# Kernel tuning notes

Measured on AMD Instinct MI355X. Metric: run time of the kernel, lower is better.

Reference implementation:

```python
import jax, jax.numpy as jnp
import numpy as np

SIZE = 384  # output resolution
SCALE = (0.8, 1.0)


def _bilinear_crop_resize(img, cs, top, left):
    """img: [C,H,W]; cs/top/left: int32 scalars. Crop [top:top+cs, left:left+cs],
    resize to SIZE x SIZE with bilinear, align_corners=False (PyTorch semantics)."""
    csf = cs.astype(jnp.float32)
    # source coords within the crop, clamped like PyTorch (src = max(src,0), upper bounded)
    coords = (jnp.arange(SIZE, dtype=jnp.float32) + 0.5) * (csf / SIZE) - 0.5
    coords = jnp.clip(coords, 0.0, csf - 1.0)
    i0 = jnp.floor(coords).astype(jnp.int32)
    i1 = jnp.minimum(i0 + 1, cs - 1)
    w = coords - i0.astype(jnp.float32)  # [SIZE]
    y0, y1 = i0 + top, i1 + top
    x0, x1 = i0 + left, i1 + left
    wy, wx = w[:, None], w[None, :]
    g = lambda yy, xx: img[:, yy[:, None], xx[None, :]]  # [C,SIZE,SIZE]
    return (g(y0, x0) * (1 - wy) * (1 - wx)
            + g(y0, x1) * (1 - wy) * wx
            + g(y1, x0) * wy * (1 - wx)
            + g(y1, x1) * wy * wx)


def _nearest_crop_resize(msk, cs, top, left):
    """msk: [1,H,W]. PyTorch mode='nearest': src_idx = floor(dst * in/out)."""
    idx = jnp.floor(jnp.arange(SIZE, dtype=jnp.float32) * cs.astype(jnp.float32) / SIZE).astype(jnp.int32)
    idx = jnp.minimum(idx, cs - 1)
    y, x = idx + top, idx + left
    return msk[:, y[:, None], x[None, :]]


def setup_inputs() -> dict:
    key = jax.random.key(0)
    k1, k2, k3, k4, k5 = jax.random.split(key, 5)
    B, C, H, W = 32, 3, 512, 512
    image = jax.random.normal(k1, (B, C, H, W), dtype=jnp.float32)
    mask = (jax.random.uniform(k2, (B, 1, H, W)) > 0.5).astype(jnp.float32)
    scale = jax.random.uniform(k3, (B,), minval=SCALE[0], maxval=SCALE[1])
    crop_size = (scale * min(H, W)).astype(jnp.int32)
    max_y = (H - crop_size).astype(jnp.float32)
    max_x = (W - crop_size).astype(jnp.float32)
    top = jnp.where(max_y > 0, jnp.floor(jax.random.uniform(k4, (B,)) * max_y), 0.0).astype(jnp.int32)
    left = jnp.where(max_x > 0, jnp.floor(jax.random.uniform(k5, (B,)) * max_x), 0.0).astype(jnp.int32)
    return {"image": image, "mask": mask, "crop_size": crop_size, "top": top, "left": left}


def reference(image, mask, crop_size, top, left):
    img_out = jax.vmap(_bilinear_crop_resize)(image, crop_size, top, left)
    msk_out = jax.vmap(_nearest_crop_resize)(mask, crop_size, top, left)
    return img_out, msk_out
```

## Files before the change

kernel.cpp:

```cpp
#include <hip/hip_runtime.h>


constexpr int OUT = 384;
constexpr int H = 512;
constexpr int W = 512;
constexpr int B = 32;
constexpr int C = 3;
constexpr int RPB = 4;
constexpr int GPB = OUT / RPB;
constexpr int SW  = 128;
constexpr int NSTRIPE = OUT / SW;
constexpr int NSLOT = 6;
constexpr int LROWS = C * NSLOT;
constexpr int NW  = 176;
constexpr int NCH = NW / 4;
constexpr int TOT_CHUNK = LROWS * NCH;
constexpr int NBLK = B * GPB * NSTRIPE;
constexpr int BPX  = NBLK / 8;

typedef float f32x4 __attribute__((ext_vector_type(4)));

__global__ __launch_bounds__(128, 6) void rrc_pair_kernel(
    const float* __restrict__ image,
    const float* __restrict__ mask,
    const int* __restrict__ crop_size,
    const int* __restrict__ top,
    const int* __restrict__ left,
    float* __restrict__ img_out,
    float* __restrict__ msk_out)
{
    __shared__ float lds[LROWS * NW + 8];

    const int hw = blockIdx.x;
    const int logical = (hw & 7) * BPX + (hw >> 3);
    const int b   = logical / (GPB * NSTRIPE);
    const int rem = logical % (GPB * NSTRIPE);
    const int grp = rem / NSTRIPE;
    const int st  = rem % NSTRIPE;
    const int i0  = grp * RPB;
    const int c0  = st * SW;
    const int tid = (int)threadIdx.x;
    const int j   = c0 + tid;

    const int cs = crop_size[b];
    const int t  = top[b];
    const int l  = left[b];
    const float csf = (float)cs;
    const float s   = csf / (float)OUT;

    float cy0 = ((float)i0 + 0.5f) * s - 0.5f;
    cy0 = fminf(fmaxf(cy0, 0.0f), csf - 1.0f);
    const int base_y = (int)floorf(cy0);

    float cx0 = ((float)c0 + 0.5f) * s - 0.5f;
    cx0 = fminf(fmaxf(cx0, 0.0f), csf - 1.0f);
    const int gx0 = (int)floorf(cx0);
    const int cbg = min(l + gx0, W - NW) & ~3;

    const float* imgb = image + (size_t)b * C * H * W;

    #pragma unroll
    for (int rd = 0; rd < 7; ++rd) {
        const int q = rd * 128 + tid;
        if (q < TOT_CHUNK) {
            const int r   = q / NCH;
            const int col = (q - r * NCH) * 4;
            const int c    = r / NSLOT;
            const int slot = r - c * NSLOT;
            const int y = min(t + base_y + slot, H - 1);
            const float* src = imgb + ((size_t)(c * H + y)) * W + cbg + col;
            __builtin_amdgcn_global_load_lds(
                (const __attribute__((address_space(1))) void*)src,
                (__attribute__((address_space(3))) void*)&lds[q * 4],
                16, 0, 0);
        }
    }
    if (tid < 8) lds[LROWS * NW + tid] = 0.0f;

    float cx = ((float)j + 0.5f) * s - 0.5f;
    cx = fminf(fmaxf(cx, 0.0f), csf - 1.0f);
    const int   ix0 = (int)floorf(cx);
    const float wx  = cx - (float)ix0;
    const int   xoff = l + ix0 - cbg;

    const int mx = min((j * cs) / OUT, cs - 1) + l;

    float mval[RPB];
    #pragma unroll
    for (int r4 = 0; r4 < RPB; ++r4) {
        int my = min(((i0 + r4) * cs) / OUT, cs - 1);
        mval[r4] = mask[((size_t)b * H + (size_t)(my + t)) * W + mx];
    }

    __syncthreads();

    #pragma unroll
    for (int r4 = 0; r4 < RPB; ++r4) {
        const int i = i0 + r4;
        float cy = ((float)i + 0.5f) * s - 0.5f;
        cy = fminf(fmaxf(cy, 0.0f), csf - 1.0f);
        int   iy0 = (int)floorf(cy);
        int   iy1 = min(iy0 + 1, cs - 1);
        float wy  = cy - (float)iy0;
        const int slot0 = iy0 - base_y;
        const int slot1 = min(iy1 - base_y, NSLOT - 1);

        const float w00 = (1.0f - wy) * (1.0f - wx);
        const float w01 = (1.0f - wy) * wx;
        const float w10 = wy * (1.0f - wx);
        const float w11 = wy * wx;

        const size_t o_base = (size_t)b * C * OUT * OUT + (size_t)i * OUT + (size_t)j;

        #pragma unroll
        for (int c = 0; c < C; ++c) {
            const float* rA = &lds[(c * NSLOT + slot0) * NW + xoff];
            const float* rB = &lds[(c * NSLOT + slot1) * NW + xoff];
            float v00 = rA[0], v01 = rA[1];
            float v10 = rB[0], v11 = rB[1];
            float rr = v00 * w00 + v01 * w01 + v10 * w10 + v11 * w11;
            __builtin_nontemporal_store(rr, img_out + o_base + (size_t)c * OUT * OUT);
        }
        __builtin_nontemporal_store(mval[r4],
            msk_out + (size_t)b * OUT * OUT + (size_t)i * OUT + (size_t)j);
    }
}

extern "C" void kernel_launch(void* const* d_in, const int* in_sizes, int n_in,
                              void* d_out, int out_size, void* d_ws, size_t ws_size,
                              hipStream_t stream) {
    const float* image = (const float*)d_in[0];
    const float* mask  = (const float*)d_in[1];
    const int* cs      = (const int*)d_in[2];
    const int* top     = (const int*)d_in[3];
    const int* left    = (const int*)d_in[4];

    float* img_out = (float*)d_out;
    float* msk_out = img_out + (size_t)B * C * OUT * OUT;

    dim3 block(128);
    dim3 grid(NBLK);
    hipLaunchKernelGGL(rrc_pair_kernel, grid, block, 0, stream,
                       image, mask, cs, top, left, img_out, msk_out);
}
```

Baseline: 31.79 us.

## Halve rows per block and have each thread emit two adjacent pixels

Each block now covers 2 output rows instead of 4, so it stages 4 source rows per channel instead of 6. The 128 threads are split into two 64-lane halves, one per row, and each thread computes two neighbouring columns and writes them with float2 stores. Occupancy is raised to 8 blocks per CU. This doubles the grid size and re-reads more overlapping source rows across blocks, in exchange for smaller LDS use, more blocks resident per CU and wider stores.

```diff
diff --git a/kernel.cpp b/kernel.cpp
--- a/kernel.cpp
+++ b/kernel.cpp
@@ -6,11 +6,11 @@
 constexpr int W = 512;
 constexpr int B = 32;
 constexpr int C = 3;
-constexpr int RPB = 4;
+constexpr int RPB = 2;
 constexpr int GPB = OUT / RPB;
 constexpr int SW  = 128;
 constexpr int NSTRIPE = OUT / SW;
-constexpr int NSLOT = 6;
+constexpr int NSLOT = 4;
 constexpr int LROWS = C * NSLOT;
 constexpr int NW  = 176;
 constexpr int NCH = NW / 4;
@@ -18,9 +18,9 @@
 constexpr int NBLK = B * GPB * NSTRIPE;
 constexpr int BPX  = NBLK / 8;
 
-typedef float f32x4 __attribute__((ext_vector_type(4)));
+typedef float f32x2 __attribute__((ext_vector_type(2)));
 
-__global__ __launch_bounds__(128, 6) void rrc_pair_kernel(
+__global__ __launch_bounds__(128, 8) void rrc_pair_kernel(
     const float* __restrict__ image,
     const float* __restrict__ mask,
     const int* __restrict__ crop_size,
@@ -29,7 +29,7 @@
     float* __restrict__ img_out,
     float* __restrict__ msk_out)
 {
-    __shared__ float lds[LROWS * NW + 8];
+    __shared__ float lds[LROWS * NW];
 
     const int hw = blockIdx.x;
     const int logical = (hw & 7) * BPX + (hw >> 3);
@@ -40,7 +40,6 @@
     const int i0  = grp * RPB;
     const int c0  = st * SW;
     const int tid = (int)threadIdx.x;
-    const int j   = c0 + tid;
 
     const int cs = crop_size[b];
     const int t  = top[b];
@@ -60,7 +59,7 @@
     const float* imgb = image + (size_t)b * C * H * W;
 
     #pragma unroll
-    for (int rd = 0; rd < 7; ++rd) {
+    for (int rd = 0; rd < 5; ++rd) {
         const int q = rd * 128 + tid;
         if (q < TOT_CHUNK) {
             const int r   = q / NCH;
@@ -75,55 +74,64 @@
                 16, 0, 0);
         }
     }
-    if (tid < 8) lds[LROWS * NW + tid] = 0.0f;
 
-    float cx = ((float)j + 0.5f) * s - 0.5f;
-    cx = fminf(fmaxf(cx, 0.0f), csf - 1.0f);
-    const int   ix0 = (int)floorf(cx);
-    const float wx  = cx - (float)ix0;
-    const int   xoff = l + ix0 - cbg;
+    const int lane = tid & 63;
+    const int i  = i0 + (tid >> 6);
+    const int j0 = c0 + 2 * lane;
 
-    const int mx = min((j * cs) / OUT, cs - 1) + l;
+    int   xo[2];
+    float wxa[2];
+    #pragma unroll
+    for (int k = 0; k < 2; ++k) {
+        float cx = ((float)(j0 + k) + 0.5f) * s - 0.5f;
+        cx = fminf(fmaxf(cx, 0.0f), csf - 1.0f);
+        int ix0 = (int)floorf(cx);
+        wxa[k] = cx - (float)ix0;
+        xo[k]  = l + ix0 - cbg;
+    }
 
-    float mval[RPB];
+    float cy = ((float)i + 0.5f) * s - 0.5f;
+    cy = fminf(fmaxf(cy, 0.0f), csf - 1.0f);
+    int   iy0 = (int)floorf(cy);
+    int   iy1 = min(iy0 + 1, cs - 1);
+    float wy  = cy - (float)iy0;
+    const int slot0 = iy0 - base_y;
+    const int slot1 = min(iy1 - base_y, NSLOT - 1);
+
+    int my = min((i * cs) / OUT, cs - 1);
+    const float* mrow = mask + ((size_t)b * H + (size_t)(my + t)) * W;
+    f32x2 mv;
     #pragma unroll
-    for (int r4 = 0; r4 < RPB; ++r4) {
-        int my = min(((i0 + r4) * cs) / OUT, cs - 1);
-        mval[r4] = mask[((size_t)b * H + (size_t)(my + t)) * W + mx];
+    for (int k = 0; k < 2; ++k) {
+        int mx = min(((j0 + k) * cs) / OUT, cs - 1);
+        mv[k] = mrow[mx + l];
     }
 
     __syncthreads();
 
+    const float w00a[2] = { (1.0f - wy) * (1.0f - wxa[0]), (1.0f - wy) * (1.0f - wxa[1]) };
+    const float w01a[2] = { (1.0f - wy) * wxa[0],          (1.0f - wy) * wxa[1] };
+    const float w10a[2] = { wy * (1.0f - wxa[0]),          wy * (1.0f - wxa[1]) };
+    const float w11a[2] = { wy * wxa[0],                   wy * wxa[1] };
+
+    const size_t o_base = (size_t)b * C * OUT * OUT + (size_t)i * OUT + (size_t)j0;
+
     #pragma unroll
-    for (int r4 = 0; r4 < RPB; ++r4) {
-        const int i = i0 + r4;
-        float cy = ((float)i + 0.5f) * s - 0.5f;
-        cy = fminf(fmaxf(cy, 0.0f), csf - 1.0f);
-        int   iy0 = (int)floorf(cy);
-        int   iy1 = min(iy0 + 1, cs - 1);
-        float wy  = cy - (float)iy0;
-        const int slot0 = iy0 - base_y;
-        const int slot1 = min(iy1 - base_y, NSLOT - 1);
+    for (int c = 0; c < C; ++c) {
+        const float* rA = &lds[(c * NSLOT + slot0) * NW];
+        const float* rB = &lds[(c * NSLOT + slot1) * NW];
+        f32x2 o;
+        #pragma unroll
+        for (int k = 0; k < 2; ++k) {
+            float v00 = rA[xo[k]], v01 = rA[xo[k] + 1];
+            float v10 = rB[xo[k]], v11 = rB[xo[k] + 1];
+            o[k] = v00 * w00a[k] + v01 * w01a[k] + v10 * w10a[k] + v11 * w11a[k];
+        }
+        __builtin_nontemporal_store(o, (f32x2*)(img_out + o_base + (size_t)c * OUT * OUT));
+    }
 
-        const float w00 = (1.0f - wy) * (1.0f - wx);
-        const float w01 = (1.0f - wy) * wx;
-        const float w10 = wy * (1.0f - wx);
-        const float w11 = wy * wx;
-
-        const size_t o_base = (size_t)b * C * OUT * OUT + (size_t)i * OUT + (size_t)j;
-
-        #pragma unroll
-        for (int c = 0; c < C; ++c) {
-            const float* rA = &lds[(c * NSLOT + slot0) * NW + xoff];
-            const float* rB = &lds[(c * NSLOT + slot1) * NW + xoff];
-            float v00 = rA[0], v01 = rA[1];
-            float v10 = rB[0], v11 = rB[1];
-            float rr = v00 * w00 + v01 * w01 + v10 * w10 + v11 * w11;
-            __builtin_nontemporal_store(rr, img_out + o_base + (size_t)c * OUT * OUT);
-        }
-        __builtin_nontemporal_store(mval[r4],
-            msk_out + (size_t)b * OUT * OUT + (size_t)i * OUT + (size_t)j);
-    }
+    __builtin_nontemporal_store(mv,
+        (f32x2*)(msk_out + (size_t)b * OUT * OUT + (size_t)i * OUT + (size_t)j0));
 }
 
 extern "C" void kernel_launch(void* const* d_in, const int* in_sizes, int n_in,
```

After: 31.76 us. About the same (-0.1%).
